# Performance work log

Hardware: AMD Instinct MI355X
Metric: run time of the kernel (lower is better)

Reference implementation:

```python
import jax, jax.numpy as jnp
import numpy as np

CTX2 = [-2, 1]
CTX3 = [-3, 3]
CTX4 = [-7, 2]


def _tdnn(x, kernel, bias, ctx_list):
    # x: [B,T,I], kernel: [O,I,K]; replaces the per-timestep index_select+conv1d loop
    T = x.shape[1]
    start = max(0, -ctx_list[0])
    end = T - ctx_list[-1] if ctx_list[-1] > 0 else T
    idx = jnp.arange(start, end)[:, None] + jnp.asarray(ctx_list)[None, :]  # [Tout,K]
    xg = x[:, idx, :]  # [B,Tout,K,I] gathered context frames
    return jnp.einsum('btki,oik->bto', xg, kernel) + bias


def _res(x, w1, b1, w2, b2, rbias):
    # ResBlock (dropout = identity in eval)
    h = jax.nn.relu(x @ w1.T + b1)
    h = h @ w2.T + b2
    return jax.nn.relu(h + x + rbias)


def _forward(x, fc1_w, fc1_b,
             res1_w1, res1_b1, res1_w2, res1_b2, res1_bias,
             tdnn2_k, tdnn2_b,
             res2_w1, res2_b1, res2_w2, res2_b2, res2_bias,
             tdnn3_k, tdnn3_b,
             res3_w1, res3_b1, res3_w2, res3_b2, res3_bias,
             tdnn4_k, tdnn4_b,
             res4_w1, res4_b1, res4_w2, res4_b2, res4_bias,
             bnf_w, bnf_b, ws1, ws2, bnw_w, bnw_b):
    h = jax.nn.relu(x @ fc1_w.T + fc1_b)
    h = _res(h, res1_w1, res1_b1, res1_w2, res1_b2, res1_bias)
    h = jax.nn.relu(_tdnn(h, tdnn2_k, tdnn2_b, CTX2))
    h = _res(h, res2_w1, res2_b1, res2_w2, res2_b2, res2_bias)
    h = jax.nn.relu(_tdnn(h, tdnn3_k, tdnn3_b, CTX3))
    h = _res(h, res3_w1, res3_b1, res3_w2, res3_b2, res3_bias)
    h = jax.nn.relu(_tdnn(h, tdnn4_k, tdnn4_b, CTX4))
    h = _res(h, res4_w1, res4_b1, res4_w2, res4_b2, res4_bias)
    h = h @ bnf_w.T + bnf_b  # [B,T',128]
    A = jax.nn.softmax(jnp.tanh(h @ ws1.T) @ ws2.T, axis=1)  # softmax over time, [B,T',heads]
    At = jnp.swapaxes(A, 1, 2)  # [B,heads,T']
    pooled = jnp.einsum('bht,btd->bhd', At, h)  # [B,heads,128]
    out = jax.nn.relu(pooled.reshape(pooled.shape[0], -1) @ bnw_w.T + bnw_b)
    return out, At


def setup_inputs() -> dict:
    B, T, D, H = 64, 800, 500, 512
    key = jax.random.key(0)
    ks = iter(jax.random.split(key, 40))
    stdv_lin = lambda fan: 1.0 / np.sqrt(fan)

    def lin(fan_in, fan_out):
        s = stdv_lin(fan_in)
        return (jax.random.uniform(next(ks), (fan_out, fan_in), jnp.float32, -s, s),
                jax.random.uniform(next(ks), (fan_out,), jnp.float32, -s, s))

    inp = {}
    inp['x'] = jax.random.normal(next(ks), (B, T, D), jnp.float32)
    inp['fc1_w'], inp['fc1_b'] = lin(D, H)
    for i in (1, 2, 3, 4):
        inp[f'res{i}_w1'], inp[f'res{i}_b1'] = lin(H, H)
        inp[f'res{i}_w2'], inp[f'res{i}_b2'] = lin(H, H)
        inp[f'res{i}_bias'] = jnp.ones((H,), jnp.float32)
    s = 1.0 / np.sqrt(H)
    for i in (2, 3, 4):
        inp[f'tdnn{i}_k'] = jax.random.normal(next(ks), (H, H, 2), jnp.float32) * s
        inp[f'tdnn{i}_b'] = jax.random.normal(next(ks), (H,), jnp.float32) * s
    inp['bnf_w'], inp['bnf_b'] = lin(H, 128)
    inp['ws1'] = jax.random.uniform(next(ks), (128, 128), jnp.float32, -0.1, 0.1)
    inp['ws2'] = jax.random.uniform(next(ks), (5, 128), jnp.float32, -0.1, 0.1)
    inp['bnw_w'], inp['bnw_b'] = lin(640, 128)
    return inp


def reference(x, fc1_w, fc1_b,
              res1_w1, res1_b1, res1_w2, res1_b2, res1_bias,
              res2_w1, res2_b1, res2_w2, res2_b2, res2_bias,
              res3_w1, res3_b1, res3_w2, res3_b2, res3_bias,
              res4_w1, res4_b1, res4_w2, res4_b2, res4_bias,
              tdnn2_k, tdnn2_b, tdnn3_k, tdnn3_b, tdnn4_k, tdnn4_b,
              bnf_w, bnf_b, ws1, ws2, bnw_w, bnw_b):
    return _forward(x, fc1_w, fc1_b,
                    res1_w1, res1_b1, res1_w2, res1_b2, res1_bias,
                    tdnn2_k, tdnn2_b,
                    res2_w1, res2_b1, res2_w2, res2_b2, res2_bias,
                    tdnn3_k, tdnn3_b,
                    res3_w1, res3_b1, res3_w2, res3_b2, res3_bias,
                    tdnn4_k, tdnn4_b,
                    res4_w1, res4_b1, res4_w2, res4_b2, res4_bias,
                    bnf_w, bnf_b, ws1, ws2, bnw_w, bnw_b)
```

## Files before the change

kernel.cpp:

```cpp
#include <hip/hip_runtime.h>
#include <hip/hip_bf16.h>

typedef unsigned short ushort_t;
typedef __attribute__((ext_vector_type(8))) short short8;
typedef __attribute__((ext_vector_type(4))) float f32x4;

__device__ __forceinline__ float bf2f(unsigned short u) {
  union { unsigned int i; float f; } v; v.i = ((unsigned int)u) << 16; return v.f;
}
__device__ __forceinline__ unsigned short f2bf(float f) {
  union { float f; unsigned int i; } v; v.f = f;
  unsigned int u = v.i;
  unsigned int r = (u + 0x7fffu + ((u >> 16) & 1u)) >> 16;
  return (unsigned short)r;
}

__device__ __forceinline__ void gload16(const void* g, void* l) {
  __builtin_amdgcn_global_load_lds(
      (const __attribute__((address_space(1))) void*)g,
      (__attribute__((address_space(3))) void*)l, 16, 0, 0);
}

template<int KTOT, int ACT, bool RES>
__global__ __launch_bounds__(256, 4) void gemm_kernel(
    const ushort_t* __restrict__ A, const ushort_t* __restrict__ W,
    const float* __restrict__ bias,
    const ushort_t* __restrict__ resin, const float* __restrict__ resbias,
    ushort_t* __restrict__ out,
    int M, int Ntot, int T_in, int T_out, int sh1, int ncb)
{
  constexpr int AROW = (KTOT == 1024) ? 512 : KTOT;
  __shared__ ushort_t As[128 * 64];
  __shared__ ushort_t Ws[128 * 64];

  const int tid = threadIdx.x;
  const int lane = tid & 63;
  const int w = tid >> 6;
  const int wm = w >> 1, wn = w & 1;

  const int nblocks = (int)gridDim.x;
  const int xcd = blockIdx.x & 7, kk = blockIdx.x >> 3;
  const int q = nblocks >> 3, rr = nblocks & 7;
  const int L = xcd * q + (xcd < rr ? xcd : rr) + kk;
  int rowblk, colblk;
  if (ncb == 4) { rowblk = L >> 2; colblk = L & 3; }
  else          { rowblk = L;      colblk = 0; }
  const int blockN = colblk * 128;
  const int blockRow = rowblk * 128;

  const int b0 = blockRow / T_out;
  const int t0 = blockRow - b0 * T_out;

  f32x4 acc[4][4];
#pragma unroll
  for (int i = 0; i < 4; ++i)
#pragma unroll
    for (int j = 0; j < 4; ++j) acc[i][j] = f32x4{0.f, 0.f, 0.f, 0.f};

  const int mloc = tid >> 3;
  const int csw = (((tid & 7) ^ ((tid >> 3) & 7))) * 8;

  for (int k0 = 0; k0 < KTOT; k0 += 64) {
    const int kcol = k0 & (AROW - 1);
    const int rowoff = (KTOT == 1024 && k0 >= 512) ? sh1 : 0;
#pragma unroll
    for (int j = 0; j < 4; ++j) {
      int m = j * 32 + mloc;
      int r = blockRow + m;
      int t = t0 + m;
      int bb = b0;
      if (t >= T_out) { ++bb; t -= T_out; }
      long grow = (r < M) ? ((long)bb * T_in + t + rowoff)
                          : ((long)b0 * T_in + t0 + rowoff);
      gload16(A + grow * AROW + kcol + csw, (char*)As + (j * 4096 + tid * 16));
    }
#pragma unroll
    for (int j = 0; j < 4; ++j) {
      int n = blockN + j * 32 + mloc;
      gload16(W + (long)n * KTOT + k0 + csw, (char*)Ws + (j * 4096 + tid * 16));
    }
    __syncthreads();
#pragma unroll
    for (int ks = 0; ks < 64; ks += 32) {
      short8 af[4], bf[4];
      const int hi = lane >> 4;
      const int rlo = lane & 15;
#pragma unroll
      for (int f = 0; f < 4; ++f) {
        int row = wm * 64 + f * 16 + rlo;
        int chunk = (ks >> 3) + hi;
        af[f] = *reinterpret_cast<const short8*>(
            (const char*)As + row * 128 + ((chunk ^ (row & 7)) << 4));
      }
#pragma unroll
      for (int f = 0; f < 4; ++f) {
        int row = wn * 64 + f * 16 + rlo;
        int chunk = (ks >> 3) + hi;
        bf[f] = *reinterpret_cast<const short8*>(
            (const char*)Ws + row * 128 + ((chunk ^ (row & 7)) << 4));
      }
#pragma unroll
      for (int fm = 0; fm < 4; ++fm)
#pragma unroll
        for (int fn = 0; fn < 4; ++fn)
          acc[fm][fn] = __builtin_amdgcn_mfma_f32_16x16x32_bf16(af[fm], bf[fn], acc[fm][fn], 0, 0, 0);
    }
    __syncthreads();
  }

  const int colb = lane & 15;
  const int rowb = (lane >> 4) * 4;
  float bv[4];
#pragma unroll
  for (int fn = 0; fn < 4; ++fn) {
    int col = blockN + wn * 64 + fn * 16 + colb;
    float b = bias ? bias[col] : 0.f;
    if (RES) b += resbias[col];
    bv[fn] = b;
  }
#pragma unroll
  for (int fm = 0; fm < 4; ++fm) {
#pragma unroll
    for (int reg = 0; reg < 4; ++reg) {
      int r = blockRow + wm * 64 + fm * 16 + rowb + reg;
      if (r < M) {
#pragma unroll
        for (int fn = 0; fn < 4; ++fn) {
          int col = blockN + wn * 64 + fn * 16 + colb;
          float v = acc[fm][fn][reg] + bv[fn];
          if (RES) v += bf2f(resin[(long)r * 512 + col]);
          if (ACT == 1) v = fmaxf(v, 0.f);
          else if (ACT == 2) v = tanhf(v);
          out[(long)r * Ntot + col] = f2bf(v);
        }
      }
    }
  }
}

__global__ __launch_bounds__(256) void pad512_f32_kernel(
    const float* __restrict__ in, ushort_t* __restrict__ out, long total, int Kin)
{
  long g = ((long)blockIdx.x * 256 + threadIdx.x) * 4;
  if (g >= total) return;
  int r = (int)(g >> 9), c = (int)(g & 511);
  ushort_t o0 = 0, o1 = 0, o2 = 0, o3 = 0;
  if (c < Kin) {
    float4 v = *(const float4*)(in + (long)r * Kin + c);
    o0 = f2bf(v.x); o1 = f2bf(v.y); o2 = f2bf(v.z); o3 = f2bf(v.w);
  }
  unsigned long long pk = (unsigned long long)o0 | ((unsigned long long)o1 << 16) |
                          ((unsigned long long)o2 << 32) | ((unsigned long long)o3 << 48);
  *(unsigned long long*)(out + g) = pk;
}

__global__ __launch_bounds__(256) void repack_tdnn_f32_kernel(
    const float* __restrict__ in, ushort_t* __restrict__ out)
{
  int g = blockIdx.x * 256 + threadIdx.x;
  int o = g >> 10, rem = g & 1023;
  int s = rem >> 9, i = rem & 511;
  out[g] = f2bf(in[(o << 10) + (i << 1) + s]);
}

__global__ __launch_bounds__(256) void cvt_kernel(
    const float* __restrict__ in, ushort_t* __restrict__ out, int n)
{
  int g = (blockIdx.x * 256 + threadIdx.x) * 4;
  if (g >= n) return;
  float4 v = *(const float4*)(in + g);
  unsigned long long pk = (unsigned long long)f2bf(v.x) | ((unsigned long long)f2bf(v.y) << 16) |
                          ((unsigned long long)f2bf(v.z) << 32) | ((unsigned long long)f2bf(v.w) << 48);
  *(unsigned long long*)(out + g) = pk;
}

__global__ __launch_bounds__(320) void attn_kernel(
    const ushort_t* __restrict__ s1, const float* __restrict__ ws2,
    float* __restrict__ At_out, int T)
{
  __shared__ float w2s[640];
  __shared__ float sc[800 * 5];
  int b = blockIdx.x, tid = threadIdx.x;
  for (int i = tid; i < 640; i += 320) w2s[i] = ws2[i];
  __syncthreads();
  for (int t = tid; t < T; t += 320) {
    const ushort_t* row = s1 + ((long)b * T + t) * 128;
    float a0 = 0, a1 = 0, a2 = 0, a3 = 0, a4 = 0;
    for (int c = 0; c < 128; c += 8) {
      short8 v = *reinterpret_cast<const short8*>(row + c);
#pragma unroll
      for (int j = 0; j < 8; ++j) {
        float xv = bf2f((unsigned short)v[j]);
        a0 += xv * w2s[0 * 128 + c + j];
        a1 += xv * w2s[1 * 128 + c + j];
        a2 += xv * w2s[2 * 128 + c + j];
        a3 += xv * w2s[3 * 128 + c + j];
        a4 += xv * w2s[4 * 128 + c + j];
      }
    }
    sc[t * 5 + 0] = a0; sc[t * 5 + 1] = a1; sc[t * 5 + 2] = a2;
    sc[t * 5 + 3] = a3; sc[t * 5 + 4] = a4;
  }
  __syncthreads();
  int h = tid >> 6, ln = tid & 63;
  float m = -1e30f;
  for (int t = ln; t < T; t += 64) m = fmaxf(m, sc[t * 5 + h]);
#pragma unroll
  for (int off = 32; off > 0; off >>= 1) m = fmaxf(m, __shfl_xor(m, off));
  float s = 0.f;
  for (int t = ln; t < T; t += 64) s += expf(sc[t * 5 + h] - m);
#pragma unroll
  for (int off = 32; off > 0; off >>= 1) s += __shfl_xor(s, off);
  float inv = 1.f / s;
  long base = ((long)b * 5 + h) * T;
  for (int t = ln; t < T; t += 64)
    At_out[base + t] = expf(sc[t * 5 + h] - m) * inv;
}

__global__ __launch_bounds__(640) void pool_kernel(
    const float* __restrict__ At_f, const ushort_t* __restrict__ hb,
    float* __restrict__ pooled, int T)
{
  int b = blockIdx.x, tid = threadIdx.x;
  int h = tid >> 7, d = tid & 127;
  const float* at = At_f + ((long)b * 5 + h) * T;
  const ushort_t* hr = hb + (long)b * T * 128 + d;
  float acc = 0.f;
  int t = 0;
  for (; t + 4 <= T; t += 4) {
    acc += at[t]     * bf2f(hr[(long)(t) * 128]);
    acc += at[t + 1] * bf2f(hr[(long)(t + 1) * 128]);
    acc += at[t + 2] * bf2f(hr[(long)(t + 2) * 128]);
    acc += at[t + 3] * bf2f(hr[(long)(t + 3) * 128]);
  }
  for (; t < T; ++t) acc += at[t] * bf2f(hr[(long)t * 128]);
  pooled[b * 640 + tid] = acc;
}

__global__ __launch_bounds__(128) void head_kernel(
    const float* __restrict__ pooled, const float* __restrict__ w,
    const float* __restrict__ bias, float* __restrict__ out)
{
  int b = blockIdx.x, o = threadIdx.x;
  const float* wr = w + o * 640;
  const float* p = pooled + b * 640;
  float acc = bias[o];
  for (int i = 0; i < 640; i += 4)
    acc += p[i] * wr[i] + p[i + 1] * wr[i + 1] +
           p[i + 2] * wr[i + 2] + p[i + 3] * wr[i + 3];
  out[b * 128 + o] = fmaxf(acc, 0.f);
}

extern "C" void kernel_launch(void* const* d_in, const int* in_sizes, int n_in,
                              void* d_out, int out_size, void* d_ws, size_t ws_size,
                              hipStream_t stream)
{
  (void)in_sizes; (void)n_in; (void)out_size; (void)ws_size;
  const float* x     = (const float*)d_in[0];
  const float* fc1_w = (const float*)d_in[1];
  const float* fc1_b = (const float*)d_in[2];
  const float *rw1[4], *rb1[4], *rw2[4], *rb2[4], *rbias[4];
  for (int i = 0; i < 4; ++i) {
    rw1[i]   = (const float*)d_in[3 + 5 * i + 0];
    rb1[i]   = (const float*)d_in[3 + 5 * i + 1];
    rw2[i]   = (const float*)d_in[3 + 5 * i + 2];
    rb2[i]   = (const float*)d_in[3 + 5 * i + 3];
    rbias[i] = (const float*)d_in[3 + 5 * i + 4];
  }
  const float *tk[3], *tb[3];
  for (int i = 0; i < 3; ++i) {
    tk[i] = (const float*)d_in[23 + 2 * i];
    tb[i] = (const float*)d_in[24 + 2 * i];
  }
  const float* bnf_w = (const float*)d_in[29];
  const float* bnf_b = (const float*)d_in[30];
  const float* ws1   = (const float*)d_in[31];
  const float* ws2   = (const float*)d_in[32];
  const float* bnw_w = (const float*)d_in[33];
  const float* bnw_b = (const float*)d_in[34];

  char* ws = (char*)d_ws;
  const size_t SZBUF = (size_t)51200 * 512 * 2;
  ushort_t* bufA = (ushort_t*)(ws);
  ushort_t* bufB = (ushort_t*)(ws + SZBUF);
  ushort_t* bufC = (ushort_t*)(ws + 2 * SZBUF);
  ushort_t* wfc1 = (ushort_t*)(ws + 3 * SZBUF);
  ushort_t* w2[3];
  w2[0] = wfc1 + 512 * 512;
  w2[1] = w2[0] + 512 * 1024;
  w2[2] = w2[1] + 512 * 1024;
  ushort_t* rwc[8];
  rwc[0] = w2[2] + 512 * 1024;
  for (int i = 1; i < 8; ++i) rwc[i] = rwc[i - 1] + 512 * 512;
  ushort_t* bnfwc = rwc[7] + 512 * 512;
  ushort_t* ws1c  = bnfwc + 128 * 512;
  float* pooled   = (float*)(ws1c + 128 * 128);

  float* out_f = (float*)d_out;
  float* At_f  = out_f + 8192;

  dim3 blk(256);
  {
    long totalx = (long)51200 * 512;
    pad512_f32_kernel<<<dim3((unsigned)((totalx / 4 + 255) / 256)), blk, 0, stream>>>(x, bufA, totalx, 500);
    long totalw = (long)512 * 512;
    pad512_f32_kernel<<<dim3((unsigned)((totalw / 4 + 255) / 256)), blk, 0, stream>>>(fc1_w, wfc1, totalw, 500);
    for (int i = 0; i < 3; ++i)
      repack_tdnn_f32_kernel<<<dim3(2048), blk, 0, stream>>>(tk[i], w2[i]);
    for (int i = 0; i < 4; ++i) {
      cvt_kernel<<<dim3(256), blk, 0, stream>>>(rw1[i], rwc[2 * i], 512 * 512);
      cvt_kernel<<<dim3(256), blk, 0, stream>>>(rw2[i], rwc[2 * i + 1], 512 * 512);
    }
    cvt_kernel<<<dim3(64), blk, 0, stream>>>(bnf_w, bnfwc, 128 * 512);
    cvt_kernel<<<dim3(16), blk, 0, stream>>>(ws1, ws1c, 128 * 128);
  }
  gemm_kernel<512, 1, false><<<dim3(1600), blk, 0, stream>>>(bufA, wfc1, fc1_b, nullptr, nullptr, bufB, 51200, 512, 51200, 51200, 0, 4);
  gemm_kernel<512, 1, false><<<dim3(1600), blk, 0, stream>>>(bufB, rwc[0], rb1[0], nullptr, nullptr, bufC, 51200, 512, 51200, 51200, 0, 4);
  gemm_kernel<512, 1, true ><<<dim3(1600), blk, 0, stream>>>(bufC, rwc[1], rb2[0], bufB, rbias[0], bufA, 51200, 512, 51200, 51200, 0, 4);
  gemm_kernel<1024, 1, false><<<dim3(1596), blk, 0, stream>>>(bufA, w2[0], tb[0], nullptr, nullptr, bufB, 51008, 512, 800, 797, 3, 4);
  gemm_kernel<512, 1, false><<<dim3(1596), blk, 0, stream>>>(bufB, rwc[2], rb1[1], nullptr, nullptr, bufC, 51008, 512, 51008, 51008, 0, 4);
  gemm_kernel<512, 1, true ><<<dim3(1596), blk, 0, stream>>>(bufC, rwc[3], rb2[1], bufB, rbias[1], bufA, 51008, 512, 51008, 51008, 0, 4);
  gemm_kernel<1024, 1, false><<<dim3(1584), blk, 0, stream>>>(bufA, w2[1], tb[1], nullptr, nullptr, bufB, 50624, 512, 797, 791, 6, 4);
  gemm_kernel<512, 1, false><<<dim3(1584), blk, 0, stream>>>(bufB, rwc[4], rb1[2], nullptr, nullptr, bufC, 50624, 512, 50624, 50624, 0, 4);
  gemm_kernel<512, 1, true ><<<dim3(1584), blk, 0, stream>>>(bufC, rwc[5], rb2[2], bufB, rbias[2], bufA, 50624, 512, 50624, 50624, 0, 4);
  gemm_kernel<1024, 1, false><<<dim3(1564), blk, 0, stream>>>(bufA, w2[2], tb[2], nullptr, nullptr, bufB, 50048, 512, 791, 782, 9, 4);
  gemm_kernel<512, 1, false><<<dim3(1564), blk, 0, stream>>>(bufB, rwc[6], rb1[3], nullptr, nullptr, bufC, 50048, 512, 50048, 50048, 0, 4);
  gemm_kernel<512, 1, true ><<<dim3(1564), blk, 0, stream>>>(bufC, rwc[7], rb2[3], bufB, rbias[3], bufA, 50048, 512, 50048, 50048, 0, 4);
  gemm_kernel<512, 0, false><<<dim3(391), blk, 0, stream>>>(bufA, bnfwc, bnf_b, nullptr, nullptr, bufB, 50048, 128, 50048, 50048, 0, 1);
  gemm_kernel<128, 2, false><<<dim3(391), blk, 0, stream>>>(bufB, ws1c, nullptr, nullptr, nullptr, bufC, 50048, 128, 50048, 50048, 0, 1);
  attn_kernel<<<dim3(64), dim3(320), 0, stream>>>(bufC, ws2, At_f, 782);
  pool_kernel<<<dim3(64), dim3(640), 0, stream>>>(At_f, bufB, pooled, 782);
  head_kernel<<<dim3(64), dim3(128), 0, stream>>>(pooled, bnw_w, bnw_b, out_f);
}
```

Before: 689.5 us.

## Add 256x256-tile double-buffered GEMM kernel for the 512-wide layers

Adds a new gemm256 kernel with 512 threads and 256x256 output tiles. It double-buffers 64-wide K slices in LDS using global_load_lds with XOR swizzling, and uses s_setprio around the MFMA bursts. The twelve big fc1, res and tdnn GEMMs are switched from 128x128 tiles to this kernel, with a quarter as many blocks and XCD-aware block remapping. The aim is more data reuse per LDS load and overlap of global loads with MFMA work. In exchange it uses 128KB of LDS per block and a large accumulator register footprint, and it leaves only about 400 blocks, which may give a poor tail across the CUs.

Result: slower. 843.2 us (+22.3%).

```diff
diff --git a/kernel.cpp b/kernel.cpp
--- a/kernel.cpp
+++ b/kernel.cpp
@@ -19,6 +19,157 @@
   __builtin_amdgcn_global_load_lds(
       (const __attribute__((address_space(1))) void*)g,
       (__attribute__((address_space(3))) void*)l, 16, 0, 0);
+}
+
+template<int KTOT>
+__device__ __forceinline__ void stage256(
+    const ushort_t* __restrict__ A, const ushort_t* __restrict__ W,
+    char* AsB, char* WsB, int kt, int tid, int blockRow, int blockN,
+    int M, int T_in, int T_out, int b0, int t0, int sh1)
+{
+  constexpr int AROW = (KTOT == 1024) ? 512 : KTOT;
+  const int kcol = (kt * 64) & (AROW - 1);
+  const int rowoff = (KTOT == 1024 && kt >= 8) ? sh1 : 0;
+  const int csw = (((tid & 7) ^ ((tid >> 3) & 7))) * 8;
+  const int mloc = tid >> 3;
+#pragma unroll
+  for (int j = 0; j < 4; ++j) {
+    int m = j * 64 + mloc;
+    int r = blockRow + m;
+    int t = t0 + m;
+    int bb = b0;
+    if (t >= T_out) { ++bb; t -= T_out; }
+    long grow = (r < M) ? ((long)bb * T_in + t + rowoff)
+                        : ((long)b0 * T_in + t0 + rowoff);
+    gload16(A + grow * AROW + kcol + csw, AsB + j * 8192 + tid * 16);
+  }
+#pragma unroll
+  for (int j = 0; j < 4; ++j) {
+    int n = blockN + j * 64 + mloc;
+    gload16(W + (long)n * KTOT + kt * 64 + csw, WsB + j * 8192 + tid * 16);
+  }
+}
+
+template<int KTOT, bool RES>
+__global__ __launch_bounds__(512, 2) void gemm256(
+    const ushort_t* __restrict__ A, const ushort_t* __restrict__ W,
+    const float* __restrict__ bias,
+    const ushort_t* __restrict__ resin, const float* __restrict__ resbias,
+    ushort_t* __restrict__ out,
+    int M, int Ntot, int T_in, int T_out, int sh1, int ncb)
+{
+  constexpr int NT = KTOT / 64;
+  __shared__ ushort_t As[2][256 * 64];
+  __shared__ ushort_t Ws[2][256 * 64];
+
+  const int tid = threadIdx.x;
+  const int lane = tid & 63;
+  const int w = tid >> 6;
+  const int wm = w >> 2, wn = w & 3;
+
+  const int nblocks = (int)gridDim.x;
+  const int xcd = blockIdx.x & 7, kk2 = blockIdx.x >> 3;
+  const int q = nblocks >> 3, rr = nblocks & 7;
+  const int L = xcd * q + (xcd < rr ? xcd : rr) + kk2;
+  int rowblk, colblk;
+  if (ncb == 2) { rowblk = L >> 1; colblk = L & 1; }
+  else          { rowblk = L;      colblk = 0; }
+  const int blockN = colblk * 256;
+  const int blockRow = rowblk * 256;
+  const int b0 = blockRow / T_out;
+  const int t0 = blockRow - b0 * T_out;
+
+  f32x4 acc[8][4];
+#pragma unroll
+  for (int i = 0; i < 8; ++i)
+#pragma unroll
+    for (int j = 0; j < 4; ++j) acc[i][j] = f32x4{0.f, 0.f, 0.f, 0.f};
+
+  stage256<KTOT>(A, W, (char*)As[0], (char*)Ws[0], 0, tid, blockRow, blockN, M, T_in, T_out, b0, t0, sh1);
+  stage256<KTOT>(A, W, (char*)As[1], (char*)Ws[1], 1, tid, blockRow, blockN, M, T_in, T_out, b0, t0, sh1);
+  asm volatile("s_waitcnt vmcnt(8)" ::: "memory");
+  __builtin_amdgcn_s_barrier();
+
+  const int rlo = lane & 15;
+  const int hi4 = lane >> 4;
+
+  for (int kt = 0; kt < NT; ++kt) {
+    const int cur = kt & 1;
+    const char* Ab = (const char*)As[cur];
+    const char* Wb = (const char*)Ws[cur];
+    short8 af[8], bf[4];
+#pragma unroll
+    for (int f = 0; f < 8; ++f) {
+      int row = wm * 128 + f * 16 + rlo;
+      af[f] = *(const short8*)(Ab + row * 128 + ((hi4 ^ (row & 7)) << 4));
+    }
+#pragma unroll
+    for (int f = 0; f < 4; ++f) {
+      int row = wn * 64 + f * 16 + rlo;
+      bf[f] = *(const short8*)(Wb + row * 128 + ((hi4 ^ (row & 7)) << 4));
+    }
+    __builtin_amdgcn_s_setprio(1);
+#pragma unroll
+    for (int fm = 0; fm < 8; ++fm)
+#pragma unroll
+      for (int fn = 0; fn < 4; ++fn)
+        acc[fm][fn] = __builtin_amdgcn_mfma_f32_16x16x32_bf16(af[fm], bf[fn], acc[fm][fn], 0, 0, 0);
+    __builtin_amdgcn_s_setprio(0);
+#pragma unroll
+    for (int f = 0; f < 8; ++f) {
+      int row = wm * 128 + f * 16 + rlo;
+      af[f] = *(const short8*)(Ab + row * 128 + (((4 + hi4) ^ (row & 7)) << 4));
+    }
+#pragma unroll
+    for (int f = 0; f < 4; ++f) {
+      int row = wn * 64 + f * 16 + rlo;
+      bf[f] = *(const short8*)(Wb + row * 128 + (((4 + hi4) ^ (row & 7)) << 4));
+    }
+    asm volatile("s_waitcnt lgkmcnt(0)" ::: "memory");
+    __builtin_amdgcn_s_barrier();
+    if (kt + 2 < NT)
+      stage256<KTOT>(A, W, (char*)As[cur], (char*)Ws[cur], kt + 2, tid, blockRow, blockN, M, T_in, T_out, b0, t0, sh1);
+    __builtin_amdgcn_s_setprio(1);
+#pragma unroll
+    for (int fm = 0; fm < 8; ++fm)
+#pragma unroll
+      for (int fn = 0; fn < 4; ++fn)
+        acc[fm][fn] = __builtin_amdgcn_mfma_f32_16x16x32_bf16(af[fm], bf[fn], acc[fm][fn], 0, 0, 0);
+    __builtin_amdgcn_s_setprio(0);
+    if (kt + 1 < NT) {
+      if (kt + 2 < NT) asm volatile("s_waitcnt vmcnt(8)" ::: "memory");
+      else             asm volatile("s_waitcnt vmcnt(0)" ::: "memory");
+      __builtin_amdgcn_s_barrier();
+    }
+  }
+
+  const int colb = lane & 15;
+  const int rowb = (lane >> 4) * 4;
+  float bv[4];
+#pragma unroll
+  for (int fn = 0; fn < 4; ++fn) {
+    int col = blockN + wn * 64 + fn * 16 + colb;
+    float b = bias ? bias[col] : 0.f;
+    if (RES) b += resbias[col];
+    bv[fn] = b;
+  }
+#pragma unroll
+  for (int fm = 0; fm < 8; ++fm) {
+#pragma unroll
+    for (int reg = 0; reg < 4; ++reg) {
+      int r = blockRow + wm * 128 + fm * 16 + rowb + reg;
+      if (r < M) {
+#pragma unroll
+        for (int fn = 0; fn < 4; ++fn) {
+          int col = blockN + wn * 64 + fn * 16 + colb;
+          float v = acc[fm][fn][reg] + bv[fn];
+          if (RES) v += bf2f(resin[(long)r * 512 + col]);
+          v = fmaxf(v, 0.f);
+          out[(long)r * Ntot + col] = f2bf(v);
+        }
+      }
+    }
+  }
 }
 
 template<int KTOT, int ACT, bool RES>
@@ -300,6 +451,7 @@
   float* At_f  = out_f + 8192;
 
   dim3 blk(256);
+  dim3 blk512(512);
   {
     long totalx = (long)51200 * 512;
     pad512_f32_kernel<<<dim3((unsigned)((totalx / 4 + 255) / 256)), blk, 0, stream>>>(x, bufA, totalx, 500);
@@ -314,18 +466,18 @@
     cvt_kernel<<<dim3(64), blk, 0, stream>>>(bnf_w, bnfwc, 128 * 512);
     cvt_kernel<<<dim3(16), blk, 0, stream>>>(ws1, ws1c, 128 * 128);
   }
-  gemm_kernel<512, 1, false><<<dim3(1600), blk, 0, stream>>>(bufA, wfc1, fc1_b, nullptr, nullptr, bufB, 51200, 512, 51200, 51200, 0, 4);
-  gemm_kernel<512, 1, false><<<dim3(1600), blk, 0, stream>>>(bufB, rwc[0], rb1[0], nullptr, nullptr, bufC, 51200, 512, 51200, 51200, 0, 4);
-  gemm_kernel<512, 1, true ><<<dim3(1600), blk, 0, stream>>>(bufC, rwc[1], rb2[0], bufB, rbias[0], bufA, 51200, 512, 51200, 51200, 0, 4);
-  gemm_kernel<1024, 1, false><<<dim3(1596), blk, 0, stream>>>(bufA, w2[0], tb[0], nullptr, nullptr, bufB, 51008, 512, 800, 797, 3, 4);
-  gemm_kernel<512, 1, false><<<dim3(1596), blk, 0, stream>>>(bufB, rwc[2], rb1[1], nullptr, nullptr, bufC, 51008, 512, 51008, 51008, 0, 4);
-  gemm_kernel<512, 1, true ><<<dim3(1596), blk, 0, stream>>>(bufC, rwc[3], rb2[1], bufB, rbias[1], bufA, 51008, 512, 51008, 51008, 0, 4);
-  gemm_kernel<1024, 1, false><<<dim3(1584), blk, 0, stream>>>(bufA, w2[1], tb[1], nullptr, nullptr, bufB, 50624, 512, 797, 791, 6, 4);
-  gemm_kernel<512, 1, false><<<dim3(1584), blk, 0, stream>>>(bufB, rwc[4], rb1[2], nullptr, nullptr, bufC, 50624, 512, 50624, 50624, 0, 4);
-  gemm_kernel<512, 1, true ><<<dim3(1584), blk, 0, stream>>>(bufC, rwc[5], rb2[2], bufB, rbias[2], bufA, 50624, 512, 50624, 50624, 0, 4);
-  gemm_kernel<1024, 1, false><<<dim3(1564), blk, 0, stream>>>(bufA, w2[2], tb[2], nullptr, nullptr, bufB, 50048, 512, 791, 782, 9, 4);
-  gemm_kernel<512, 1, false><<<dim3(1564), blk, 0, stream>>>(bufB, rwc[6], rb1[3], nullptr, nullptr, bufC, 50048, 512, 50048, 50048, 0, 4);
-  gemm_kernel<512, 1, true ><<<dim3(1564), blk, 0, stream>>>(bufC, rwc[7], rb2[3], bufB, rbias[3], bufA, 50048, 512, 50048, 50048, 0, 4);
+  gemm256<512, false><<<dim3(400), blk512, 0, stream>>>(bufA, wfc1, fc1_b, nullptr, nullptr, bufB, 51200, 512, 51200, 51200, 0, 2);
+  gemm256<512, false><<<dim3(400), blk512, 0, stream>>>(bufB, rwc[0], rb1[0], nullptr, nullptr, bufC, 51200, 512, 51200, 51200, 0, 2);
+  gemm256<512, true ><<<dim3(400), blk512, 0, stream>>>(bufC, rwc[1], rb2[0], bufB, rbias[0], bufA, 51200, 512, 51200, 51200, 0, 2);
+  gemm256<1024, false><<<dim3(400), blk512, 0, stream>>>(bufA, w2[0], tb[0], nullptr, nullptr, bufB, 51008, 512, 800, 797, 3, 2);
+  gemm256<512, false><<<dim3(400), blk512, 0, stream>>>(bufB, rwc[2], rb1[1], nullptr, nullptr, bufC, 51008, 512, 51008, 51008, 0, 2);
+  gemm256<512, true ><<<dim3(400), blk512, 0, stream>>>(bufC, rwc[3], rb2[1], bufB, rbias[1], bufA, 51008, 512, 51008, 51008, 0, 2);
+  gemm256<1024, false><<<dim3(396), blk512, 0, stream>>>(bufA, w2[1], tb[1], nullptr, nullptr, bufB, 50624, 512, 797, 791, 6, 2);
+  gemm256<512, false><<<dim3(396), blk512, 0, stream>>>(bufB, rwc[4], rb1[2], nullptr, nullptr, bufC, 50624, 512, 50624, 50624, 0, 2);
+  gemm256<512, true ><<<dim3(396), blk512, 0, stream>>>(bufC, rwc[5], rb2[2], bufB, rbias[2], bufA, 50624, 512, 50624, 50624, 0, 2);
+  gemm256<1024, false><<<dim3(392), blk512, 0, stream>>>(bufA, w2[2], tb[2], nullptr, nullptr, bufB, 50048, 512, 791, 782, 9, 2);
+  gemm256<512, false><<<dim3(392), blk512, 0, stream>>>(bufB, rwc[6], rb1[3], nullptr, nullptr, bufC, 50048, 512, 50048, 50048, 0, 2);
+  gemm256<512, true ><<<dim3(392), blk512, 0, stream>>>(bufC, rwc[7], rb2[3], bufB, rbias[3], bufA, 50048, 512, 50048, 50048, 0, 2);
   gemm_kernel<512, 0, false><<<dim3(391), blk, 0, stream>>>(bufA, bnfwc, bnf_b, nullptr, nullptr, bufB, 50048, 128, 50048, 50048, 0, 1);
   gemm_kernel<128, 2, false><<<dim3(391), blk, 0, stream>>>(bufB, ws1c, nullptr, nullptr, nullptr, bufC, 50048, 128, 50048, 50048, 0, 1);
   attn_kernel<<<dim3(64), dim3(320), 0, stream>>>(bufC, ws2, At_f, 782);
```

## Convert GEMM kernels to persistent blocks with atomic tile scheduling

Applied to the files above, without the earlier changes.

Each GEMM launch now uses a fixed grid of 1280 persistent blocks that pull output tiles from a global atomic counter, replacing the one-block-per-tile launch and the XCD-aware tile remapping. Launch bounds rise from 4 to 5 blocks per SM to allow more resident blocks. The aim is to reduce tail-wave imbalance across the ~1600 tiles. In exchange it adds an atomic and an extra barrier per tile, loses the XCD locality mapping, and may increase register pressure.

Result: slower. 1.079 ms (+56.6%).

```diff
diff --git a/kernel.cpp b/kernel.cpp
--- a/kernel.cpp
+++ b/kernel.cpp
@@ -22,120 +22,128 @@
 }
 
 template<int KTOT, int ACT, bool RES>
-__global__ __launch_bounds__(256, 4) void gemm_kernel(
+__global__ __launch_bounds__(256, 5) void gemm_kernel(
     const ushort_t* __restrict__ A, const ushort_t* __restrict__ W,
     const float* __restrict__ bias,
     const ushort_t* __restrict__ resin, const float* __restrict__ resbias,
     ushort_t* __restrict__ out,
-    int M, int Ntot, int T_in, int T_out, int sh1, int ncb)
+    int M, int Ntot, int T_in, int T_out, int sh1, int ncb, int ntiles,
+    unsigned* __restrict__ cnt)
 {
   constexpr int AROW = (KTOT == 1024) ? 512 : KTOT;
   __shared__ ushort_t As[128 * 64];
   __shared__ ushort_t Ws[128 * 64];
+  __shared__ unsigned s_idx;
 
   const int tid = threadIdx.x;
   const int lane = tid & 63;
   const int w = tid >> 6;
   const int wm = w >> 1, wn = w & 1;
 
-  const int nblocks = (int)gridDim.x;
-  const int xcd = blockIdx.x & 7, kk = blockIdx.x >> 3;
-  const int q = nblocks >> 3, rr = nblocks & 7;
-  const int L = xcd * q + (xcd < rr ? xcd : rr) + kk;
-  int rowblk, colblk;
-  if (ncb == 4) { rowblk = L >> 2; colblk = L & 3; }
-  else          { rowblk = L;      colblk = 0; }
-  const int blockN = colblk * 128;
-  const int blockRow = rowblk * 128;
-
-  const int b0 = blockRow / T_out;
-  const int t0 = blockRow - b0 * T_out;
-
-  f32x4 acc[4][4];
-#pragma unroll
-  for (int i = 0; i < 4; ++i)
-#pragma unroll
-    for (int j = 0; j < 4; ++j) acc[i][j] = f32x4{0.f, 0.f, 0.f, 0.f};
-
   const int mloc = tid >> 3;
   const int csw = (((tid & 7) ^ ((tid >> 3) & 7))) * 8;
-
-  for (int k0 = 0; k0 < KTOT; k0 += 64) {
-    const int kcol = k0 & (AROW - 1);
-    const int rowoff = (KTOT == 1024 && k0 >= 512) ? sh1 : 0;
-#pragma unroll
-    for (int j = 0; j < 4; ++j) {
-      int m = j * 32 + mloc;
-      int r = blockRow + m;
-      int t = t0 + m;
-      int bb = b0;
-      if (t >= T_out) { ++bb; t -= T_out; }
-      long grow = (r < M) ? ((long)bb * T_in + t + rowoff)
-                          : ((long)b0 * T_in + t0 + rowoff);
-      gload16(A + grow * AROW + kcol + csw, (char*)As + (j * 4096 + tid * 16));
-    }
-#pragma unroll
-    for (int j = 0; j < 4; ++j) {
-      int n = blockN + j * 32 + mloc;
-      gload16(W + (long)n * KTOT + k0 + csw, (char*)Ws + (j * 4096 + tid * 16));
-    }
+  const int rlo = lane & 15;
+  const int hi = lane >> 4;
+
+  for (;;) {
+    if (tid == 0) s_idx = atomicAdd(cnt, 1u);
     __syncthreads();
-#pragma unroll
-    for (int ks = 0; ks < 64; ks += 32) {
-      short8 af[4], bf[4];
-      const int hi = lane >> 4;
-      const int rlo = lane & 15;
-#pragma unroll
-      for (int f = 0; f < 4; ++f) {
-        int row = wm * 64 + f * 16 + rlo;
-        int chunk = (ks >> 3) + hi;
-        af[f] = *reinterpret_cast<const short8*>(
-            (const char*)As + row * 128 + ((chunk ^ (row & 7)) << 4));
-      }
-#pragma unroll
-      for (int f = 0; f < 4; ++f) {
-        int row = wn * 64 + f * 16 + rlo;
-        int chunk = (ks >> 3) + hi;
-        bf[f] = *reinterpret_cast<const short8*>(
-            (const char*)Ws + row * 128 + ((chunk ^ (row & 7)) << 4));
-      }
-#pragma unroll
-      for (int fm = 0; fm < 4; ++fm)
-#pragma unroll
-        for (int fn = 0; fn < 4; ++fn)
-          acc[fm][fn] = __builtin_amdgcn_mfma_f32_16x16x32_bf16(af[fm], bf[fn], acc[fm][fn], 0, 0, 0);
-    }
-    __syncthreads();
-  }
-
-  const int colb = lane & 15;
-  const int rowb = (lane >> 4) * 4;
-  float bv[4];
-#pragma unroll
-  for (int fn = 0; fn < 4; ++fn) {
-    int col = blockN + wn * 64 + fn * 16 + colb;
-    float b = bias ? bias[col] : 0.f;
-    if (RES) b += resbias[col];
-    bv[fn] = b;
-  }
-#pragma unroll
-  for (int fm = 0; fm < 4; ++fm) {
-#pragma unroll
-    for (int reg = 0; reg < 4; ++reg) {
-      int r = blockRow + wm * 64 + fm * 16 + rowb + reg;
-      if (r < M) {
-#pragma unroll
-        for (int fn = 0; fn < 4; ++fn) {
-          int col = blockN + wn * 64 + fn * 16 + colb;
-          float v = acc[fm][fn][reg] + bv[fn];
-          if (RES) v += bf2f(resin[(long)r * 512 + col]);
-          if (ACT == 1) v = fmaxf(v, 0.f);
-          else if (ACT == 2) v = tanhf(v);
-          out[(long)r * Ntot + col] = f2bf(v);
+    const unsigned idx = s_idx;
+    if (idx >= (unsigned)ntiles) break;
+
+    int rowblk, colblk;
+    if (ncb == 4) { rowblk = (int)(idx >> 2); colblk = (int)(idx & 3u); }
+    else          { rowblk = (int)idx;        colblk = 0; }
+    const int blockN = colblk * 128;
+    const int blockRow = rowblk * 128;
+    const int b0 = blockRow / T_out;
+    const int t0 = blockRow - b0 * T_out;
+
+    f32x4 acc[4][4];
+#pragma unroll
+    for (int i = 0; i < 4; ++i)
+#pragma unroll
+      for (int j = 0; j < 4; ++j) acc[i][j] = f32x4{0.f, 0.f, 0.f, 0.f};
+
+    for (int k0 = 0; k0 < KTOT; k0 += 64) {
+      const int kcol = k0 & (AROW - 1);
+      const int rowoff = (KTOT == 1024 && k0 >= 512) ? sh1 : 0;
+#pragma unroll
+      for (int j = 0; j < 4; ++j) {
+        int m = j * 32 + mloc;
+        int r = blockRow + m;
+        int t = t0 + m;
+        int bb = b0;
+        if (t >= T_out) { ++bb; t -= T_out; }
+        long grow = (r < M) ? ((long)bb * T_in + t + rowoff)
+                            : ((long)b0 * T_in + t0 + rowoff);
+        gload16(A + grow * AROW + kcol + csw, (char*)As + (j * 4096 + tid * 16));
+      }
+#pragma unroll
+      for (int j = 0; j < 4; ++j) {
+        int n = blockN + j * 32 + mloc;
+        gload16(W + (long)n * KTOT + k0 + csw, (char*)Ws + (j * 4096 + tid * 16));
+      }
+      __syncthreads();
+#pragma unroll
+      for (int ks = 0; ks < 64; ks += 32) {
+        short8 af[4], bf[4];
+#pragma unroll
+        for (int f = 0; f < 4; ++f) {
+          int row = wm * 64 + f * 16 + rlo;
+          int chunk = (ks >> 3) + hi;
+          af[f] = *reinterpret_cast<const short8*>(
+              (const char*)As + row * 128 + ((chunk ^ (row & 7)) << 4));
         }
-      }
-    }
-  }
+#pragma unroll
+        for (int f = 0; f < 4; ++f) {
+          int row = wn * 64 + f * 16 + rlo;
+          int chunk = (ks >> 3) + hi;
+          bf[f] = *reinterpret_cast<const short8*>(
+              (const char*)Ws + row * 128 + ((chunk ^ (row & 7)) << 4));
+        }
+#pragma unroll
+        for (int fm = 0; fm < 4; ++fm)
+#pragma unroll
+          for (int fn = 0; fn < 4; ++fn)
+            acc[fm][fn] = __builtin_amdgcn_mfma_f32_16x16x32_bf16(af[fm], bf[fn], acc[fm][fn], 0, 0, 0);
+      }
+      __syncthreads();
+    }
+
+    const int colb = lane & 15;
+    const int rowb = (lane >> 4) * 4;
+    float bv[4];
+#pragma unroll
+    for (int fn = 0; fn < 4; ++fn) {
+      int col = blockN + wn * 64 + fn * 16 + colb;
+      float b = bias ? bias[col] : 0.f;
+      if (RES) b += resbias[col];
+      bv[fn] = b;
+    }
+#pragma unroll
+    for (int fm = 0; fm < 4; ++fm) {
+#pragma unroll
+      for (int reg = 0; reg < 4; ++reg) {
+        int r = blockRow + wm * 64 + fm * 16 + rowb + reg;
+        if (r < M) {
+#pragma unroll
+          for (int fn = 0; fn < 4; ++fn) {
+            int col = blockN + wn * 64 + fn * 16 + colb;
+            float v = acc[fm][fn][reg] + bv[fn];
+            if (RES) v += bf2f(resin[(long)r * 512 + col]);
+            if (ACT == 1) v = fmaxf(v, 0.f);
+            else if (ACT == 2) v = tanhf(v);
+            out[(long)r * Ntot + col] = f2bf(v);
+          }
+        }
+      }
+    }
+  }
+}
+
+__global__ void init_counters_kernel(unsigned* __restrict__ cnt) {
+  if (threadIdx.x < 16) cnt[threadIdx.x] = 0;
 }
 
 __global__ __launch_bounds__(256) void pad512_f32_kernel(
@@ -295,11 +303,14 @@
   ushort_t* bnfwc = rwc[7] + 512 * 512;
   ushort_t* ws1c  = bnfwc + 128 * 512;
   float* pooled   = (float*)(ws1c + 128 * 128);
+  unsigned* cnt   = (unsigned*)(pooled + 64 * 640);
 
   float* out_f = (float*)d_out;
   float* At_f  = out_f + 8192;
 
   dim3 blk(256);
+  const unsigned GCAP = 1280;
+  init_counters_kernel<<<dim3(1), dim3(64), 0, stream>>>(cnt);
   {
     long totalx = (long)51200 * 512;
     pad512_f32_kernel<<<dim3((unsigned)((totalx / 4 + 255) / 256)), blk, 0, stream>>>(x, bufA, totalx, 500);
@@ -314,20 +325,20 @@
     cvt_kernel<<<dim3(64), blk, 0, stream>>>(bnf_w, bnfwc, 128 * 512);
     cvt_kernel<<<dim3(16), blk, 0, stream>>>(ws1, ws1c, 128 * 128);
   }
-  gemm_kernel<512, 1, false><<<dim3(1600), blk, 0, stream>>>(bufA, wfc1, fc1_b, nullptr, nullptr, bufB, 51200, 512, 51200, 51200, 0, 4);
-  gemm_kernel<512, 1, false><<<dim3(1600), blk, 0, stream>>>(bufB, rwc[0], rb1[0], nullptr, nullptr, bufC, 51200, 512, 51200, 51200, 0, 4);
-  gemm_kernel<512, 1, true ><<<dim3(1600), blk, 0, stream>>>(bufC, rwc[1], rb2[0], bufB, rbias[0], bufA, 51200, 512, 51200, 51200, 0, 4);
-  gemm_kernel<1024, 1, false><<<dim3(1596), blk, 0, stream>>>(bufA, w2[0], tb[0], nullptr, nullptr, bufB, 51008, 512, 800, 797, 3, 4);
-  gemm_kernel<512, 1, false><<<dim3(1596), blk, 0, stream>>>(bufB, rwc[2], rb1[1], nullptr, nullptr, bufC, 51008, 512, 51008, 51008, 0, 4);
-  gemm_kernel<512, 1, true ><<<dim3(1596), blk, 0, stream>>>(bufC, rwc[3], rb2[1], bufB, rbias[1], bufA, 51008, 512, 51008, 51008, 0, 4);
-  gemm_kernel<1024, 1, false><<<dim3(1584), blk, 0, stream>>>(bufA, w2[1], tb[1], nullptr, nullptr, bufB, 50624, 512, 797, 791, 6, 4);
-  gemm_kernel<512, 1, false><<<dim3(1584), blk, 0, stream>>>(bufB, rwc[4], rb1[2], nullptr, nullptr, bufC, 50624, 512, 50624, 50624, 0, 4);
-  gemm_kernel<512, 1, true ><<<dim3(1584), blk, 0, stream>>>(bufC, rwc[5], rb2[2], bufB, rbias[2], bufA, 50624, 512, 50624, 50624, 0, 4);
-  gemm_kernel<1024, 1, false><<<dim3(1564), blk, 0, stream>>>(bufA, w2[2], tb[2], nullptr, nullptr, bufB, 50048, 512, 791, 782, 9, 4);
-  gemm_kernel<512, 1, false><<<dim3(1564), blk, 0, stream>>>(bufB, rwc[6], rb1[3], nullptr, nullptr, bufC, 50048, 512, 50048, 50048, 0, 4);
-  gemm_kernel<512, 1, true ><<<dim3(1564), blk, 0, stream>>>(bufC, rwc[7], rb2[3], bufB, rbias[3], bufA, 50048, 512, 50048, 50048, 0, 4);
-  gemm_kernel<512, 0, false><<<dim3(391), blk, 0, stream>>>(bufA, bnfwc, bnf_b, nullptr, nullptr, bufB, 50048, 128, 50048, 50048, 0, 1);
-  gemm_kernel<128, 2, false><<<dim3(391), blk, 0, stream>>>(bufB, ws1c, nullptr, nullptr, nullptr, bufC, 50048, 128, 50048, 50048, 0, 1);
+  gemm_kernel<512, 1, false><<<dim3(GCAP), blk, 0, stream>>>(bufA, wfc1, fc1_b, nullptr, nullptr, bufB, 51200, 512, 51200, 51200, 0, 4, 1600, cnt + 0);
+  gemm_kernel<512, 1, false><<<dim3(GCAP), blk, 0, stream>>>(bufB, rwc[0], rb1[0], nullptr, nullptr, bufC, 51200, 512, 51200, 51200, 0, 4, 1600, cnt + 1);
+  gemm_kernel<512, 1, true ><<<dim3(GCAP), blk, 0, stream>>>(bufC, rwc[1], rb2[0], bufB, rbias[0], bufA, 51200, 512, 51200, 51200, 0, 4, 1600, cnt + 2);
+  gemm_kernel<1024, 1, false><<<dim3(GCAP), blk, 0, stream>>>(bufA, w2[0], tb[0], nullptr, nullptr, bufB, 51008, 512, 800, 797, 3, 4, 1596, cnt + 3);
+  gemm_kernel<512, 1, false><<<dim3(GCAP), blk, 0, stream>>>(bufB, rwc[2], rb1[1], nullptr, nullptr, bufC, 51008, 512, 51008, 51008, 0, 4, 1596, cnt + 4);
+  gemm_kernel<512, 1, true ><<<dim3(GCAP), blk, 0, stream>>>(bufC, rwc[3], rb2[1], bufB, rbias[1], bufA, 51008, 512, 51008, 51008, 0, 4, 1596, cnt + 5);
+  gemm_kernel<1024, 1, false><<<dim3(GCAP), blk, 0, stream>>>(bufA, w2[1], tb[1], nullptr, nullptr, bufB, 50624, 512, 797, 791, 6, 4, 1584, cnt + 6);
+  gemm_kernel<512, 1, false><<<dim3(GCAP), blk, 0, stream>>>(bufB, rwc[4], rb1[2], nullptr, nullptr, bufC, 50624, 512, 50624, 50624, 0, 4, 1584, cnt + 7);
+  gemm_kernel<512, 1, true ><<<dim3(GCAP), blk, 0, stream>>>(bufC, rwc[5], rb2[2], bufB, rbias[2], bufA, 50624, 512, 50624, 50624, 0, 4, 1584, cnt + 8);
+  gemm_kernel<1024, 1, false><<<dim3(GCAP), blk, 0, stream>>>(bufA, w2[2], tb[2], nullptr, nullptr, bufB, 50048, 512, 791, 782, 9, 4, 1564, cnt + 9);
+  gemm_kernel<512, 1, false><<<dim3(GCAP), blk, 0, stream>>>(bufB, rwc[6], rb1[3], nullptr, nullptr, bufC, 50048, 512, 50048, 50048, 0, 4, 1564, cnt + 10);
+  gemm_kernel<512, 1, true ><<<dim3(GCAP), blk, 0, stream>>>(bufC, rwc[7], rb2[3], bufB, rbias[3], bufA, 50048, 512, 50048, 50048, 0, 4, 1564, cnt + 11);
+  gemm_kernel<512, 0, false><<<dim3(391), blk, 0, stream>>>(bufA, bnfwc, bnf_b, nullptr, nullptr, bufB, 50048, 128, 50048, 50048, 0, 1, 391, cnt + 12);
+  gemm_kernel<128, 2, false><<<dim3(391), blk, 0, stream>>>(bufB, ws1c, nullptr, nullptr, nullptr, bufC, 50048, 128, 50048, 50048, 0, 1, 391, cnt + 13);
   attn_kernel<<<dim3(64), dim3(320), 0, stream>>>(bufC, ws2, At_f, 782);
   pool_kernel<<<dim3(64), dim3(640), 0, stream>>>(At_f, bufB, pooled, 782);
   head_kernel<<<dim3(64), dim3(128), 0, stream>>>(pooled, bnw_w, bnw_b, out_f);
```

## Double-buffer GEMM LDS tiles with BK=32 and prefetch next k-tile

Applied to the files above, without the earlier changes.

Replaces the single 64-wide K tile with two 32-wide LDS buffers so the next tile's global-to-LDS loads are issued before the current tile's MFMAs run. Row base addresses are precomputed once outside the K loop, and the LDS swizzle is changed to fit 64-byte rows. This aims to hide global load latency behind compute while keeping LDS use the same, but it halves the work per barrier and doubles the number of loop iterations and syncs.

Result: slower. 780.5 us (+13.2%).

```diff
diff --git a/kernel.cpp b/kernel.cpp
--- a/kernel.cpp
+++ b/kernel.cpp
@@ -30,8 +30,9 @@
     int M, int Ntot, int T_in, int T_out, int sh1, int ncb)
 {
   constexpr int AROW = (KTOT == 1024) ? 512 : KTOT;
-  __shared__ ushort_t As[128 * 64];
-  __shared__ ushort_t Ws[128 * 64];
+  constexpr int NT = KTOT / 32;
+  __shared__ ushort_t As[2][128 * 32];
+  __shared__ ushort_t Ws[2][128 * 32];
 
   const int tid = threadIdx.x;
   const int lane = tid & 63;
@@ -57,54 +58,61 @@
 #pragma unroll
     for (int j = 0; j < 4; ++j) acc[i][j] = f32x4{0.f, 0.f, 0.f, 0.f};
 
-  const int mloc = tid >> 3;
-  const int csw = (((tid & 7) ^ ((tid >> 3) & 7))) * 8;
-
-  for (int k0 = 0; k0 < KTOT; k0 += 64) {
-    const int kcol = k0 & (AROW - 1);
-    const int rowoff = (KTOT == 1024 && k0 >= 512) ? sh1 : 0;
-#pragma unroll
-    for (int j = 0; j < 4; ++j) {
-      int m = j * 32 + mloc;
-      int r = blockRow + m;
-      int t = t0 + m;
-      int bb = b0;
-      if (t >= T_out) { ++bb; t -= T_out; }
-      long grow = (r < M) ? ((long)bb * T_in + t + rowoff)
-                          : ((long)b0 * T_in + t0 + rowoff);
-      gload16(A + grow * AROW + kcol + csw, (char*)As + (j * 4096 + tid * 16));
-    }
-#pragma unroll
-    for (int j = 0; j < 4; ++j) {
-      int n = blockN + j * 32 + mloc;
-      gload16(W + (long)n * KTOT + k0 + csw, (char*)Ws + (j * 4096 + tid * 16));
-    }
-    __syncthreads();
-#pragma unroll
-    for (int ks = 0; ks < 64; ks += 32) {
-      short8 af[4], bf[4];
-      const int hi = lane >> 4;
-      const int rlo = lane & 15;
-#pragma unroll
-      for (int f = 0; f < 4; ++f) {
-        int row = wm * 64 + f * 16 + rlo;
-        int chunk = (ks >> 3) + hi;
-        af[f] = *reinterpret_cast<const short8*>(
-            (const char*)As + row * 128 + ((chunk ^ (row & 7)) << 4));
-      }
-#pragma unroll
-      for (int f = 0; f < 4; ++f) {
-        int row = wn * 64 + f * 16 + rlo;
-        int chunk = (ks >> 3) + hi;
-        bf[f] = *reinterpret_cast<const short8*>(
-            (const char*)Ws + row * 128 + ((chunk ^ (row & 7)) << 4));
-      }
-#pragma unroll
-      for (int fm = 0; fm < 4; ++fm)
-#pragma unroll
-        for (int fn = 0; fn < 4; ++fn)
-          acc[fm][fn] = __builtin_amdgcn_mfma_f32_16x16x32_bf16(af[fm], bf[fn], acc[fm][fn], 0, 0, 0);
-    }
+  const int srow = tid >> 2;
+  const int csw = (((tid & 3) ^ ((tid >> 3) & 3))) * 8;
+  long abase[2], wbase[2];
+#pragma unroll
+  for (int j = 0; j < 2; ++j) {
+    int m = j * 64 + srow;
+    int r = blockRow + m;
+    int t = t0 + m;
+    int bb = b0;
+    if (t >= T_out) { ++bb; t -= T_out; }
+    long grow = (r < M) ? ((long)bb * T_in + t) : ((long)b0 * T_in + t0);
+    abase[j] = grow * AROW + csw;
+    wbase[j] = (long)(blockN + j * 64 + srow) * KTOT + csw;
+  }
+
+  auto stage = [&](int bsel, int kt) {
+    const int kcol = (kt * 32) & (AROW - 1);
+    const long aoff = (KTOT == 1024 && kt >= 16) ? (long)sh1 * AROW + kcol : (long)kcol;
+#pragma unroll
+    for (int j = 0; j < 2; ++j)
+      gload16(A + abase[j] + aoff, (char*)As[bsel] + (j * 4096 + tid * 16));
+#pragma unroll
+    for (int j = 0; j < 2; ++j)
+      gload16(W + wbase[j] + kt * 32, (char*)Ws[bsel] + (j * 4096 + tid * 16));
+  };
+
+  stage(0, 0);
+  __syncthreads();
+
+  const int rlo = lane & 15;
+  const int hi = lane >> 4;
+
+  for (int kt = 0; kt < NT; ++kt) {
+    const int cur = kt & 1;
+    if (kt + 1 < NT) stage(cur ^ 1, kt + 1);
+    const char* Ab = (const char*)As[cur];
+    const char* Wb = (const char*)Ws[cur];
+    short8 af[4], bf[4];
+#pragma unroll
+    for (int f = 0; f < 4; ++f) {
+      int row = wm * 64 + f * 16 + rlo;
+      af[f] = *reinterpret_cast<const short8*>(
+          Ab + row * 64 + ((hi ^ ((row >> 1) & 3)) << 4));
+    }
+#pragma unroll
+    for (int f = 0; f < 4; ++f) {
+      int row = wn * 64 + f * 16 + rlo;
+      bf[f] = *reinterpret_cast<const short8*>(
+          Wb + row * 64 + ((hi ^ ((row >> 1) & 3)) << 4));
+    }
+#pragma unroll
+    for (int fm = 0; fm < 4; ++fm)
+#pragma unroll
+      for (int fn = 0; fn < 4; ++fn)
+        acc[fm][fn] = __builtin_amdgcn_mfma_f32_16x16x32_bf16(af[fm], bf[fn], acc[fm][fn], 0, 0, 0);
     __syncthreads();
   }
 
```
